# Kernel tuning notes

Measured on AMD Instinct MI355X. Metric: run time of the kernel, lower is better.

Reference implementation:

```python
import jax, jax.numpy as jnp
import numpy as np

BNK, L, DIN, DOUT, NREL = 1280, 64, 512, 256, 40

def setup_inputs() -> dict:
    key = jax.random.key(0)
    ks = jax.random.split(key, 10)
    rep = jax.random.normal(ks[0], (BNK, L, DIN), dtype=jnp.float32)
    # adj_arc_in[..., 0] = flattened sentence index, adj_arc_in[..., 1] = head token position
    sent = jnp.broadcast_to(jnp.arange(BNK, dtype=jnp.int64)[:, None], (BNK, L))
    head = jax.random.randint(ks[1], (BNK, L), 0, L, dtype=jnp.int64)
    adj_arc_in = jnp.stack([sent, head], axis=-1)  # [BNK, L, 2]
    adj_lab_in = jax.random.randint(ks[2], (BNK, L), 0, NREL, dtype=jnp.int64)
    adj_mask_in = (jax.random.uniform(ks[3], (BNK, L)) < 0.9).astype(jnp.float32)
    adj_mask_loop = jnp.ones((BNK, L), dtype=jnp.float32)
    mask = jnp.ones((BNK, L), dtype=jnp.float32)
    # parameters (xavier-ish init)
    W_in = jax.random.normal(ks[4], (DIN, DOUT), dtype=jnp.float32) * (2.0 / (DIN + DOUT)) ** 0.5
    b_in = jnp.zeros((NREL, DOUT), dtype=jnp.float32)
    W_gate_in = jax.random.uniform(ks[5], (DIN, 1), dtype=jnp.float32)
    b_gate_in = jnp.ones((NREL, 1), dtype=jnp.float32)
    W_self = jax.random.normal(ks[6], (DIN, DOUT), dtype=jnp.float32) * (2.0 / (DIN + DOUT)) ** 0.5
    W_gate_self = jax.random.uniform(ks[7], (DIN, 1), dtype=jnp.float32)
    return {"rep": rep, "adj_mask_in": adj_mask_in, "adj_mask_loop": adj_mask_loop,
            "mask": mask, "W_in": W_in, "b_in": b_in, "W_gate_in": W_gate_in,
            "b_gate_in": b_gate_in, "W_self": W_self, "W_gate_self": W_gate_self,
            "adj_arc_in": adj_arc_in, "adj_lab_in": adj_lab_in}

def reference(rep, adj_mask_in, adj_mask_loop, mask, W_in, b_in, W_gate_in,
              b_gate_in, W_self, W_gate_self, adj_arc_in, adj_lab_in):
    bnk, l, din = rep.shape
    dout = W_in.shape[1]
    rep_ = rep.reshape(bnk * l, din)                    # [M, Din]
    idx = adj_arc_in[..., 0].reshape(-1) * l + adj_arc_in[..., 1].reshape(-1)  # [M]
    lab = adj_lab_in.reshape(-1)                        # [M]
    # in-arc potential: gather projected head token, add relation-typed bias
    in_pot = (rep_ @ W_in)[idx] + b_in[lab]             # [M, Dout]
    in_gate = (rep_ @ W_gate_in)[idx, 0] + b_gate_in[lab, 0]  # [M]
    # self-loop potential
    self_pot = rep_ @ W_self                            # [M, Dout]
    self_gate = (rep_ @ W_gate_self)[:, 0]              # [M]
    pots = jnp.stack([in_pot, self_pot], axis=1)        # [M, 2, Dout]
    gates = jnp.stack([in_gate, self_gate], axis=1)     # [M, 2]
    msoft = jnp.stack([adj_mask_in.reshape(-1), adj_mask_loop.reshape(-1)], axis=1)  # [M, 2]
    # original multiplies by mask_soft twice: potentials * mask_soft * (sigmoid(gate) * mask_soft)
    w = jax.nn.sigmoid(gates) * msoft * msoft           # [M, 2]
    res = jax.nn.relu(jnp.einsum('mdk,md->mk', pots, w))  # [M, Dout]
    res = res.reshape(bnk, l, dout) * mask.reshape(bnk, l)[..., None]
    return res
```

## Files before the change

### kernel.cpp

```cpp
#include <hip/hip_runtime.h>


#define BNK   1280
#define LTOK  64
#define DIN   512
#define DOUT  256
#define TPB   1024
#define PSTR  264

#define SMEM_BYTES 73472

typedef __attribute__((ext_vector_type(4))) float f32x4;
typedef __attribute__((ext_vector_type(8))) short s16x8;

__device__ __forceinline__ unsigned short f2bf(float f) {
  unsigned u = __float_as_uint(f);
  unsigned r = (u + 0x7FFFu + ((u >> 16) & 1u)) >> 16;
  return (unsigned short)r;
}
__device__ __forceinline__ float bf2f(unsigned short h) {
  return __uint_as_float(((unsigned)h) << 16);
}
__device__ __forceinline__ float sigmoidf_(float x) {
  return 1.0f / (1.0f + __expf(-x));
}

__global__ __launch_bounds__(256) void wprep_kernel(const float* __restrict__ W_in,
                                                    const float* __restrict__ W_self,
                                                    unsigned short* __restrict__ Wt) {
  __shared__ float tile[32][33];
  const int t  = threadIdx.x;
  const int c0 = (blockIdx.x & 15) * 32;
  const int k0 = (blockIdx.x >> 4) * 32;
  const float* src = (c0 < DOUT) ? W_in : W_self;
  const int cadj   = (c0 < DOUT) ? c0 : (c0 - DOUT);
  {
    const int kk = t >> 3;
    const int cc = (t & 7) * 4;
    const float4 v = *(const float4*)(src + (size_t)(k0 + kk) * DOUT + cadj + cc);
    tile[kk][cc + 0] = v.x; tile[kk][cc + 1] = v.y;
    tile[kk][cc + 2] = v.z; tile[kk][cc + 3] = v.w;
  }
  __syncthreads();
  {
    const int cc = t >> 3;
    const int kk = (t & 7) * 4;
    ushort4 o;
    o.x = f2bf(tile[kk + 0][cc]); o.y = f2bf(tile[kk + 1][cc]);
    o.z = f2bf(tile[kk + 2][cc]); o.w = f2bf(tile[kk + 3][cc]);
    *(ushort4*)(Wt + (size_t)(c0 + cc) * DIN + k0 + kk) = o;
  }
}

__global__ __launch_bounds__(TPB, 4) void gcn_kernel(
    const float* __restrict__ rep,
    const float* __restrict__ adj_mask_in,
    const float* __restrict__ adj_mask_loop,
    const float* __restrict__ maskp,
    const float* __restrict__ b_in,
    const float* __restrict__ w_gate_in,
    const float* __restrict__ b_gate_in,
    const float* __restrict__ w_gate_self,
    const int* __restrict__ arc,
    const int* __restrict__ lab,
    const unsigned short* __restrict__ Wt,
    float* __restrict__ out)
{
  __shared__ __align__(16) char smem[SMEM_BYTES];
  unsigned short* As  = (unsigned short*)(smem);
  unsigned short* Pin = (unsigned short*)(smem);
  unsigned short* Psf = (unsigned short*)(smem + 33792);
  float* wgi  = (float*)(smem + 67584);
  float* wgs  = (float*)(smem + 69632);
  float* gld  = (float*)(smem + 71680);
  float* winl = (float*)(smem + 72192);
  float* wsfl = (float*)(smem + 72448);
  float* mskl = (float*)(smem + 72704);
  int*   hdl  = (int*)(smem + 72960);
  int*   lbl  = (int*)(smem + 73216);

  const int b    = blockIdx.x;
  const int t    = threadIdx.x;
  const int w    = t >> 6;
  const int lane = t & 63;
  const int nlo  = lane & 15;
  const int quad = lane >> 4;

  if (t < DIN) {
    wgi[t] = w_gate_in[t];
    wgs[t] = w_gate_self[t];
  }
  __syncthreads();

  {
    const int r = t >> 4, p = t & 15;
    const float* arow = rep + (size_t)(b * LTOK + r) * DIN;
    float si = 0.f, ss = 0.f;
    #pragma unroll
    for (int i = 0; i < 4; ++i) {
      const int kg = p + 16 * i;
      const int kb = kg * 8;
      const float4 v0 = *(const float4*)(arow + kb);
      const float4 v1 = *(const float4*)(arow + kb + 4);
      const float4 g0 = *(const float4*)(wgi + kb);
      const float4 g1 = *(const float4*)(wgi + kb + 4);
      const float4 h0 = *(const float4*)(wgs + kb);
      const float4 h1 = *(const float4*)(wgs + kb + 4);
      si += v0.x*g0.x + v0.y*g0.y + v0.z*g0.z + v0.w*g0.w
          + v1.x*g1.x + v1.y*g1.y + v1.z*g1.z + v1.w*g1.w;
      ss += v0.x*h0.x + v0.y*h0.y + v0.z*h0.z + v0.w*h0.w
          + v1.x*h1.x + v1.y*h1.y + v1.z*h1.z + v1.w*h1.w;
      s16x8 o;
      o[0] = (short)f2bf(v0.x); o[1] = (short)f2bf(v0.y);
      o[2] = (short)f2bf(v0.z); o[3] = (short)f2bf(v0.w);
      o[4] = (short)f2bf(v1.x); o[5] = (short)f2bf(v1.y);
      o[6] = (short)f2bf(v1.z); o[7] = (short)f2bf(v1.w);
      const int u = ((p >> 2) + 4 * i) * 256 + (p & 3) * 64 + (r ^ (p & 7));
      *(s16x8*)(As + u * 8) = o;
    }
    #pragma unroll
    for (int off = 1; off < 16; off <<= 1) {
      si += __shfl_xor(si, off, 64);
      ss += __shfl_xor(ss, off, 64);
    }
    if (p == 0) {
      gld[r * 2 + 0] = si;
      gld[r * 2 + 1] = ss;
    }
  }
  __syncthreads();

  f32x4 acc[4][2];
  #pragma unroll
  for (int i = 0; i < 4; ++i)
    #pragma unroll
    for (int j = 0; j < 2; ++j) {
      f32x4 z = {0.f, 0.f, 0.f, 0.f};
      acc[i][j] = z;
    }

  const unsigned short* aeven = As + (quad * 64 + (nlo ^ quad)) * 8;
  const unsigned short* aodd  = As + (quad * 64 + (nlo ^ (quad + 4))) * 8;
  const unsigned short* wb0 = Wt + (size_t)(w * 32 + nlo) * DIN + quad * 8;
  const unsigned short* wb1 = wb0 + 16 * DIN;

  s16x8 bfr[3][2];
  bfr[0][0] = *(const s16x8*)(wb0);
  bfr[0][1] = *(const s16x8*)(wb1);
  bfr[1][0] = *(const s16x8*)(wb0 + 32);
  bfr[1][1] = *(const s16x8*)(wb1 + 32);

  #pragma unroll
  for (int kc = 0; kc < 16; ++kc) {
    if (kc + 2 < 16) {
      bfr[(kc + 2) % 3][0] = *(const s16x8*)(wb0 + (kc + 2) * 32);
      bfr[(kc + 2) % 3][1] = *(const s16x8*)(wb1 + (kc + 2) * 32);
    }
    const unsigned short* ab = ((kc & 1) ? aodd : aeven) + kc * 2048;
    s16x8 af[4];
    #pragma unroll
    for (int mt = 0; mt < 4; ++mt)
      af[mt] = *(const s16x8*)(ab + mt * 128);
    __builtin_amdgcn_s_setprio(1);
    #pragma unroll
    for (int nt = 0; nt < 2; ++nt)
      #pragma unroll
      for (int mt = 0; mt < 4; ++mt)
        acc[mt][nt] = __builtin_amdgcn_mfma_f32_16x16x32_bf16(af[mt], bfr[kc % 3][nt], acc[mt][nt], 0, 0, 0);
    __builtin_amdgcn_s_setprio(0);
  }

  __syncthreads();

  if (t < LTOK) {
    const int m  = b * LTOK + t;
    const int hd = arc[2 * m + 1];
    const int lb = lab[m];
    const float am = adj_mask_in[m];
    const float al = adj_mask_loop[m];
    winl[t] = sigmoidf_(gld[hd * 2 + 0] + b_gate_in[lb]) * am * am;
    wsfl[t] = sigmoidf_(gld[t * 2 + 1]) * al * al;
    mskl[t] = maskp[m];
    hdl[t]  = hd;
    lbl[t]  = lb;
  }

  {
    unsigned short* dst = (w < 8) ? Pin : Psf;
    const int cb = (w & 7) * 32;
    #pragma unroll
    for (int mt = 0; mt < 4; ++mt)
      #pragma unroll
      for (int nt = 0; nt < 2; ++nt)
        #pragma unroll
        for (int rr = 0; rr < 4; ++rr) {
          const int row = mt * 16 + quad * 4 + rr;
          const int col = cb + nt * 16 + nlo;
          dst[row * PSTR + col] = f2bf(acc[mt][nt][rr]);
        }
  }
  __syncthreads();

  #pragma unroll
  for (int i = 0; i < 4; ++i) {
    const int q   = i * TPB + t;
    const int row = q >> 6;
    const int cl  = (q & 63) * 4;
    const int hd  = hdl[row];
    const int lb  = lbl[row];
    const float wi = winl[row], ws = wsfl[row], mk = mskl[row];
    const float4  bi = *(const float4*)(b_in + lb * DOUT + cl);
    const ushort4 pi = *(const ushort4*)(Pin + hd * PSTR + cl);
    const ushort4 ps = *(const ushort4*)(Psf + row * PSTR + cl);
    float4 v;
    v.x = (bf2f(pi.x) + bi.x) * wi + bf2f(ps.x) * ws;
    v.y = (bf2f(pi.y) + bi.y) * wi + bf2f(ps.y) * ws;
    v.z = (bf2f(pi.z) + bi.z) * wi + bf2f(ps.z) * ws;
    v.w = (bf2f(pi.w) + bi.w) * wi + bf2f(ps.w) * ws;
    v.x = fmaxf(v.x, 0.f) * mk; v.y = fmaxf(v.y, 0.f) * mk;
    v.z = fmaxf(v.z, 0.f) * mk; v.w = fmaxf(v.w, 0.f) * mk;
    *(float4*)(out + (size_t)(b * LTOK + row) * DOUT + cl) = v;
  }
}

extern "C" void kernel_launch(void* const* d_in, const int* in_sizes, int n_in,
                              void* d_out, int out_size, void* d_ws, size_t ws_size,
                              hipStream_t stream) {
  const float* rep           = (const float*)d_in[0];
  const float* adj_mask_in   = (const float*)d_in[1];
  const float* adj_mask_loop = (const float*)d_in[2];
  const float* mask          = (const float*)d_in[3];
  const float* W_in          = (const float*)d_in[4];
  const float* b_in          = (const float*)d_in[5];
  const float* W_gate_in     = (const float*)d_in[6];
  const float* b_gate_in     = (const float*)d_in[7];
  const float* W_self        = (const float*)d_in[8];
  const float* W_gate_self   = (const float*)d_in[9];
  const int*   arc           = (const int*)d_in[10];
  const int*   lab           = (const int*)d_in[11];
  float* out = (float*)d_out;
  unsigned short* Wt = (unsigned short*)d_ws;

  wprep_kernel<<<256, 256, 0, stream>>>(W_in, W_self, Wt);
  gcn_kernel<<<BNK, TPB, 0, stream>>>(rep, adj_mask_in, adj_mask_loop, mask, b_in,
                                      W_gate_in, b_gate_in, W_gate_self, arc, lab, Wt, out);
}
```

Baseline: 353.0 us.

## Split output columns across two blocks and pipeline A/B staging through LDS

Each sentence is now handled by two 512-thread blocks, each computing half of the output columns for both W_in and W_self. The K loop becomes a software pipeline: weight chunks are copied directly global-to-LDS with double buffering, and activation chunks are converted to bf16 and written into a triple-buffered swizzled LDS area one step ahead. This aims to overlap memory traffic with MFMA work and to cut LDS use for higher occupancy. In exchange, rep is read twice and the gate dot products are recomputed per half, and the pipeline relies on hand-placed waitcnt and barrier instructions.

```diff
diff --git a/kernel.cpp b/kernel.cpp
--- a/kernel.cpp
+++ b/kernel.cpp
@@ -5,10 +5,26 @@
 #define LTOK  64
 #define DIN   512
 #define DOUT  256
-#define TPB   1024
-#define PSTR  264
-
-#define SMEM_BYTES 73472
+#define NREL  40
+#define TPB   512
+#define PSTR  132
+
+#define ABUF_OFF   0
+#define BBUF_OFF   12288
+#define WGI_OFF    45056
+#define WGS_OFF    47104
+#define WINL_OFF   49152
+#define WSFL_OFF   49408
+#define MSKL_OFF   49664
+#define HDL_OFF    49920
+#define LBL_OFF    50176
+#define GLD_OFF    50432
+#define AMD_OFF    50944
+#define ALD_OFF    51200
+#define BGL_OFF    51456
+#define PIN_OFF    0
+#define PSF_OFF    16896
+#define SMEM_BYTES 51712
 
 typedef __attribute__((ext_vector_type(4))) float f32x4;
 typedef __attribute__((ext_vector_type(8))) short s16x8;
@@ -67,68 +83,75 @@
     float* __restrict__ out)
 {
   __shared__ __align__(16) char smem[SMEM_BYTES];
-  unsigned short* As  = (unsigned short*)(smem);
-  unsigned short* Pin = (unsigned short*)(smem);
-  unsigned short* Psf = (unsigned short*)(smem + 33792);
-  float* wgi  = (float*)(smem + 67584);
-  float* wgs  = (float*)(smem + 69632);
-  float* gld  = (float*)(smem + 71680);
-  float* winl = (float*)(smem + 72192);
-  float* wsfl = (float*)(smem + 72448);
-  float* mskl = (float*)(smem + 72704);
-  int*   hdl  = (int*)(smem + 72960);
-  int*   lbl  = (int*)(smem + 73216);
-
-  const int b    = blockIdx.x;
+  unsigned short* Pin = (unsigned short*)(smem + PIN_OFF);
+  unsigned short* Psf = (unsigned short*)(smem + PSF_OFF);
+  float* wgi  = (float*)(smem + WGI_OFF);
+  float* wgs  = (float*)(smem + WGS_OFF);
+  float* winl = (float*)(smem + WINL_OFF);
+  float* wsfl = (float*)(smem + WSFL_OFF);
+  float* mskl = (float*)(smem + MSKL_OFF);
+  int*   hdl  = (int*)(smem + HDL_OFF);
+  int*   lbl  = (int*)(smem + LBL_OFF);
+  float* gld  = (float*)(smem + GLD_OFF);
+  float* amd  = (float*)(smem + AMD_OFF);
+  float* ald  = (float*)(smem + ALD_OFF);
+  float* bgl  = (float*)(smem + BGL_OFF);
+
+  const int b    = blockIdx.x >> 1;
+  const int h    = blockIdx.x & 1;
   const int t    = threadIdx.x;
   const int w    = t >> 6;
   const int lane = t & 63;
   const int nlo  = lane & 15;
   const int quad = lane >> 4;
 
-  if (t < DIN) {
-    wgi[t] = w_gate_in[t];
-    wgs[t] = w_gate_self[t];
-  }
-  __syncthreads();
-
-  {
-    const int r = t >> 4, p = t & 15;
-    const float* arow = rep + (size_t)(b * LTOK + r) * DIN;
-    float si = 0.f, ss = 0.f;
-    #pragma unroll
-    for (int i = 0; i < 4; ++i) {
-      const int kg = p + 16 * i;
-      const int kb = kg * 8;
-      const float4 v0 = *(const float4*)(arow + kb);
-      const float4 v1 = *(const float4*)(arow + kb + 4);
-      const float4 g0 = *(const float4*)(wgi + kb);
-      const float4 g1 = *(const float4*)(wgi + kb + 4);
-      const float4 h0 = *(const float4*)(wgs + kb);
-      const float4 h1 = *(const float4*)(wgs + kb + 4);
-      si += v0.x*g0.x + v0.y*g0.y + v0.z*g0.z + v0.w*g0.w
-          + v1.x*g1.x + v1.y*g1.y + v1.z*g1.z + v1.w*g1.w;
-      ss += v0.x*h0.x + v0.y*h0.y + v0.z*h0.z + v0.w*h0.w
-          + v1.x*h1.x + v1.y*h1.y + v1.z*h1.z + v1.w*h1.w;
-      s16x8 o;
-      o[0] = (short)f2bf(v0.x); o[1] = (short)f2bf(v0.y);
-      o[2] = (short)f2bf(v0.z); o[3] = (short)f2bf(v0.w);
-      o[4] = (short)f2bf(v1.x); o[5] = (short)f2bf(v1.y);
-      o[6] = (short)f2bf(v1.z); o[7] = (short)f2bf(v1.w);
-      const int u = ((p >> 2) + 4 * i) * 256 + (p & 3) * 64 + (r ^ (p & 7));
-      *(s16x8*)(As + u * 8) = o;
-    }
-    #pragma unroll
-    for (int off = 1; off < 16; off <<= 1) {
-      si += __shfl_xor(si, off, 64);
-      ss += __shfl_xor(ss, off, 64);
-    }
-    if (p == 0) {
-      gld[r * 2 + 0] = si;
-      gld[r * 2 + 1] = ss;
-    }
-  }
-  __syncthreads();
+  const int r  = t >> 3;
+  const int kk = t & 7;
+  const int pa = kk >> 1;
+  const float* arow = rep + (size_t)(b * LTOK + r) * DIN + kk * 4;
+
+  const int j0 = w * 128 + lane;
+  const int j1 = j0 + 64;
+  const int c0 = j0 >> 2, p0 = j0 & 3;
+  const int c1 = j1 >> 2, p1 = j1 & 3;
+  const int cc0 = c0 + h * 128 + ((c0 >> 7) << 7);
+  const int cc1 = c1 + h * 128 + ((c1 >> 7) << 7);
+  const size_t boff0 = (size_t)cc0 * DIN + ((p0 ^ (c0 & 3)) << 3);
+  const size_t boff1 = (size_t)cc1 * DIN + ((p1 ^ (c1 & 3)) << 3);
+
+  int bofs[2];
+  #pragma unroll
+  for (int nt = 0; nt < 2; ++nt) {
+    const int c = w * 32 + nt * 16 + nlo;
+    bofs[nt] = (c * 4 + (quad ^ (c & 3))) << 4;
+  }
+
+  f32x4 Ar0, Ar1, Ar2;
+  float si = 0.f, ss = 0.f;
+
+#define AR(k) ((k) == 0 ? Ar0 : (k) == 1 ? Ar1 : Ar2)
+
+#define STAGE_B(ch) do { \
+    const unsigned short* _s0 = Wt + boff0 + (size_t)((ch) & 15) * 32; \
+    const unsigned short* _s1 = Wt + boff1 + (size_t)((ch) & 15) * 32; \
+    char* _d = smem + BBUF_OFF + (((ch) & 1) << 14); \
+    __builtin_amdgcn_global_load_lds((const __attribute__((address_space(1))) void*)_s0, \
+        (__attribute__((address_space(3))) void*)(_d + ((w * 128 + lane) << 4)), 16, 0, 0); \
+    __builtin_amdgcn_global_load_lds((const __attribute__((address_space(1))) void*)_s1, \
+        (__attribute__((address_space(3))) void*)(_d + ((w * 128 + 64 + lane) << 4)), 16, 0, 0); \
+  } while (0)
+
+#define PUT_A(ch) do { \
+    const f32x4 _v = AR((ch) % 3); \
+    const f32x4 _g = *(const f32x4*)(wgi + (ch) * 32 + kk * 4); \
+    const f32x4 _h = *(const f32x4*)(wgs + (ch) * 32 + kk * 4); \
+    si += _v[0] * _g[0] + _v[1] * _g[1] + _v[2] * _g[2] + _v[3] * _g[3]; \
+    ss += _v[0] * _h[0] + _v[1] * _h[1] + _v[2] * _h[2] + _v[3] * _h[3]; \
+    ushort4 _o; \
+    _o.x = f2bf(_v[0]); _o.y = f2bf(_v[1]); _o.z = f2bf(_v[2]); _o.w = f2bf(_v[3]); \
+    const int _u = pa * 64 + (r ^ ((((ch) & 7) << 2) + pa)); \
+    *(ushort4*)(smem + ((ch) % 3) * 4096 + _u * 16 + ((kk & 1) << 3)) = _o; \
+  } while (0)
 
   f32x4 acc[4][2];
   #pragma unroll
@@ -139,88 +162,116 @@
       acc[i][j] = z;
     }
 
-  const unsigned short* aeven = As + (quad * 64 + (nlo ^ quad)) * 8;
-  const unsigned short* aodd  = As + (quad * 64 + (nlo ^ (quad + 4))) * 8;
-  const unsigned short* wb0 = Wt + (size_t)(w * 32 + nlo) * DIN + quad * 8;
-  const unsigned short* wb1 = wb0 + 16 * DIN;
-
-  s16x8 bfr[3][2];
-  bfr[0][0] = *(const s16x8*)(wb0);
-  bfr[0][1] = *(const s16x8*)(wb1);
-  bfr[1][0] = *(const s16x8*)(wb0 + 32);
-  bfr[1][1] = *(const s16x8*)(wb1 + 32);
+  if (t < LTOK) {
+    const int m = b * LTOK + t;
+    hdl[t] = arc[2 * m + 1];
+    lbl[t] = lab[m];
+    amd[t] = adj_mask_in[m];
+    ald[t] = adj_mask_loop[m];
+    mskl[t] = maskp[m];
+  }
+  if (t < NREL) bgl[t] = b_gate_in[t];
+  wgi[t] = w_gate_in[t];
+  wgs[t] = w_gate_self[t];
+
+  STAGE_B(0);
+  asm volatile("" ::: "memory");
+  Ar0 = *(const f32x4*)(arow);
+  Ar1 = *(const f32x4*)(arow + 32);
+  asm volatile("s_waitcnt lgkmcnt(0)" ::: "memory");
+  __builtin_amdgcn_s_barrier();
+  __builtin_amdgcn_sched_barrier(0);
+  PUT_A(0);
 
   #pragma unroll
   for (int kc = 0; kc < 16; ++kc) {
-    if (kc + 2 < 16) {
-      bfr[(kc + 2) % 3][0] = *(const s16x8*)(wb0 + (kc + 2) * 32);
-      bfr[(kc + 2) % 3][1] = *(const s16x8*)(wb1 + (kc + 2) * 32);
+    if (kc < 15) STAGE_B(kc + 1);
+    if (kc == 15) {
+      asm volatile("s_waitcnt vmcnt(0)" ::: "memory");
+    } else {
+      asm volatile("s_waitcnt vmcnt(3)" ::: "memory");
     }
-    const unsigned short* ab = ((kc & 1) ? aodd : aeven) + kc * 2048;
-    s16x8 af[4];
+    asm volatile("s_waitcnt lgkmcnt(0)" ::: "memory");
+    __builtin_amdgcn_s_barrier();
+    __builtin_amdgcn_sched_barrier(0);
+
+    if (kc < 14) AR((kc + 2) % 3) = *(const f32x4*)(arow + (kc + 2) * 32);
+    if (kc < 15) PUT_A(kc + 1);
+
+    {
+      const int sw = (kc & 7) << 2;
+      const char* ab = smem + (kc % 3) * 4096;
+      const char* bb = smem + BBUF_OFF + ((kc & 1) << 14);
+      s16x8 af[4];
+      #pragma unroll
+      for (int mt = 0; mt < 4; ++mt)
+        af[mt] = *(const s16x8*)(ab + ((quad * 64 + ((mt * 16 + nlo) ^ (sw + quad))) << 4));
+      s16x8 bfv[2];
+      #pragma unroll
+      for (int nt = 0; nt < 2; ++nt)
+        bfv[nt] = *(const s16x8*)(bb + bofs[nt]);
+      __builtin_amdgcn_s_setprio(1);
+      #pragma unroll
+      for (int nt = 0; nt < 2; ++nt)
+        #pragma unroll
+        for (int mt = 0; mt < 4; ++mt)
+          acc[mt][nt] = __builtin_amdgcn_mfma_f32_16x16x32_bf16(af[mt], bfv[nt], acc[mt][nt], 0, 0, 0);
+      __builtin_amdgcn_s_setprio(0);
+    }
+    __builtin_amdgcn_sched_barrier(0);
+    __builtin_amdgcn_s_barrier();
+  }
+
+  si += __shfl_xor(si, 1, 64); si += __shfl_xor(si, 2, 64); si += __shfl_xor(si, 4, 64);
+  ss += __shfl_xor(ss, 1, 64); ss += __shfl_xor(ss, 2, 64); ss += __shfl_xor(ss, 4, 64);
+  if ((t & 7) == 0) { gld[r * 2] = si; gld[r * 2 + 1] = ss; }
+
+  asm volatile("s_waitcnt lgkmcnt(0)" ::: "memory");
+  __builtin_amdgcn_s_barrier();
+  __builtin_amdgcn_sched_barrier(0);
+
+  if (t < LTOK) {
+    winl[t] = sigmoidf_(gld[hdl[t] * 2] + bgl[lbl[t]]) * amd[t] * amd[t];
+    wsfl[t] = sigmoidf_(gld[t * 2 + 1]) * ald[t] * ald[t];
+  }
+
+  {
+    unsigned short* dst = (w < 4) ? Pin : Psf;
+    const int cb = (w & 3) * 32;
     #pragma unroll
     for (int mt = 0; mt < 4; ++mt)
-      af[mt] = *(const s16x8*)(ab + mt * 128);
-    __builtin_amdgcn_s_setprio(1);
-    #pragma unroll
-    for (int nt = 0; nt < 2; ++nt)
-      #pragma unroll
-      for (int mt = 0; mt < 4; ++mt)
-        acc[mt][nt] = __builtin_amdgcn_mfma_f32_16x16x32_bf16(af[mt], bfr[kc % 3][nt], acc[mt][nt], 0, 0, 0);
-    __builtin_amdgcn_s_setprio(0);
-  }
-
-  __syncthreads();
-
-  if (t < LTOK) {
-    const int m  = b * LTOK + t;
-    const int hd = arc[2 * m + 1];
-    const int lb = lab[m];
-    const float am = adj_mask_in[m];
-    const float al = adj_mask_loop[m];
-    winl[t] = sigmoidf_(gld[hd * 2 + 0] + b_gate_in[lb]) * am * am;
-    wsfl[t] = sigmoidf_(gld[t * 2 + 1]) * al * al;
-    mskl[t] = maskp[m];
-    hdl[t]  = hd;
-    lbl[t]  = lb;
-  }
-
-  {
-    unsigned short* dst = (w < 8) ? Pin : Psf;
-    const int cb = (w & 7) * 32;
-    #pragma unroll
-    for (int mt = 0; mt < 4; ++mt)
       #pragma unroll
       for (int nt = 0; nt < 2; ++nt)
         #pragma unroll
-        for (int rr = 0; rr < 4; ++rr) {
-          const int row = mt * 16 + quad * 4 + rr;
-          const int col = cb + nt * 16 + nlo;
-          dst[row * PSTR + col] = f2bf(acc[mt][nt][rr]);
-        }
-  }
-  __syncthreads();
+        for (int rr = 0; rr < 4; ++rr)
+          dst[(mt * 16 + quad * 4 + rr) * PSTR + cb + nt * 16 + nlo] = f2bf(acc[mt][nt][rr]);
+  }
+  asm volatile("s_waitcnt lgkmcnt(0)" ::: "memory");
+  __builtin_amdgcn_s_barrier();
 
   #pragma unroll
   for (int i = 0; i < 4; ++i) {
     const int q   = i * TPB + t;
-    const int row = q >> 6;
-    const int cl  = (q & 63) * 4;
+    const int row = q >> 5;
+    const int cl  = (q & 31) * 4;
     const int hd  = hdl[row];
     const int lb  = lbl[row];
-    const float wi = winl[row], ws = wsfl[row], mk = mskl[row];
-    const float4  bi = *(const float4*)(b_in + lb * DOUT + cl);
+    const float wi = winl[row], wsv = wsfl[row], mk = mskl[row];
+    const float4  bi = *(const float4*)(b_in + lb * DOUT + h * 128 + cl);
     const ushort4 pi = *(const ushort4*)(Pin + hd * PSTR + cl);
     const ushort4 ps = *(const ushort4*)(Psf + row * PSTR + cl);
     float4 v;
-    v.x = (bf2f(pi.x) + bi.x) * wi + bf2f(ps.x) * ws;
-    v.y = (bf2f(pi.y) + bi.y) * wi + bf2f(ps.y) * ws;
-    v.z = (bf2f(pi.z) + bi.z) * wi + bf2f(ps.z) * ws;
-    v.w = (bf2f(pi.w) + bi.w) * wi + bf2f(ps.w) * ws;
+    v.x = (bf2f(pi.x) + bi.x) * wi + bf2f(ps.x) * wsv;
+    v.y = (bf2f(pi.y) + bi.y) * wi + bf2f(ps.y) * wsv;
+    v.z = (bf2f(pi.z) + bi.z) * wi + bf2f(ps.z) * wsv;
+    v.w = (bf2f(pi.w) + bi.w) * wi + bf2f(ps.w) * wsv;
     v.x = fmaxf(v.x, 0.f) * mk; v.y = fmaxf(v.y, 0.f) * mk;
     v.z = fmaxf(v.z, 0.f) * mk; v.w = fmaxf(v.w, 0.f) * mk;
-    *(float4*)(out + (size_t)(b * LTOK + row) * DOUT + cl) = v;
-  }
+    *(float4*)(out + (size_t)(b * LTOK + row) * DOUT + h * 128 + cl) = v;
+  }
+#undef AR
+#undef STAGE_B
+#undef PUT_A
 }
 
 extern "C" void kernel_launch(void* const* d_in, const int* in_sizes, int n_in,
@@ -242,6 +293,6 @@
   unsigned short* Wt = (unsigned short*)d_ws;
 
   wprep_kernel<<<256, 256, 0, stream>>>(W_in, W_self, Wt);
-  gcn_kernel<<<BNK, TPB, 0, stream>>>(rep, adj_mask_in, adj_mask_loop, mask, b_in,
-                                      W_gate_in, b_gate_in, W_gate_self, arc, lab, Wt, out);
-}
+  gcn_kernel<<<BNK * 2, TPB, 0, stream>>>(rep, adj_mask_in, adj_mask_loop, mask, b_in,
+                                          W_gate_in, b_gate_in, W_gate_self, arc, lab, Wt, out);
+}
```

New measurement: 549.7 us. +55.7%, slower.
